# Optimization experiments

Measured on AMD Instinct MI355X. Metric: run time of the kernel, lower is better.

Reference implementation:

```python
import jax, jax.numpy as jnp
import numpy as np
from jax import lax

NUM_DISP = 64
BLOCK = 21
EPS = 1e-12  # F.normalize default eps


def _box_sum(v):
    # v: (N, H, W) -> BLOCK x BLOCK zero-padded box sum (same shape), separable.
    p = BLOCK // 2
    v = v[:, None]  # (N,1,H,W)
    kv = jnp.ones((1, 1, BLOCK, 1), v.dtype)
    kh = jnp.ones((1, 1, 1, BLOCK), v.dtype)
    v = lax.conv_general_dilated(v, kv, (1, 1), ((p, p), (0, 0)))
    v = lax.conv_general_dilated(v, kh, (1, 1), ((0, 0), (p, p)))
    return v[:, 0]


def _l2norm_c(img):
    n = jnp.sqrt(jnp.sum(img * img, axis=1, keepdims=True))
    return img / jnp.maximum(n, EPS)


def _disparity(left, right):
    # left, right: (B, 3, H, W)
    left = _l2norm_c(left)
    right = _l2norm_c(right)
    B, C, H, W = left.shape
    d = jnp.arange(NUM_DISP)
    xs = jnp.arange(W)
    idx = xs[None, :] - d[:, None]              # (D, W): source column in right image
    valid = (idx >= 0)
    r_shift = right[:, :, :, jnp.clip(idx, 0)]  # (B, C, H, D, W)
    r_shift = jnp.where(valid[None, None, None], r_shift, 0.0)
    # per-pixel channel-summed absolute difference -> (B, D, H, W)
    diff = jnp.sum(jnp.abs(left[:, :, :, None, :] - r_shift), axis=1)  # (B, H, D, W)
    diff = jnp.transpose(diff, (0, 2, 1, 3))    # (B, D, H, W)
    cost = _box_sum(diff.reshape(B * NUM_DISP, H, W)).reshape(B, NUM_DISP, H, W)
    cost = cost / (C * BLOCK * BLOCK)           # mean SAD over block elements
    return jnp.argmin(cost, axis=1).astype(left.dtype)  # (B, H, W)


def setup_inputs() -> dict:
    key = jax.random.key(0)
    k1, k2 = jax.random.split(key)
    x = jax.random.normal(k1, (2, 6, 320, 512), dtype=jnp.float32)
    gt = jax.random.normal(k2, (2, 6, 320, 512), dtype=jnp.float32)
    return {"x": x, "gt": gt}


def reference(x, gt):
    disp_gt = _disparity(gt[:, :3], gt[:, 3:])
    disp_pred = _disparity(x[:, :3], x[:, 3:])
    return jnp.mean(jnp.abs(disp_pred - disp_gt))
```

## Files before the change

### kernel.cpp

```cpp
#include <hip/hip_runtime.h>
#include <math.h>

constexpr int B = 2, H = 320, W = 512, D = 64;
constexpr int HW = H * W;
constexpr int R = 10;
constexpr int SEG = 80;
constexpr int NSEG = H / SEG;
constexpr int RS = 548;
constexpr float EPS = 1e-12f;

__global__ void k_norm(const float* __restrict__ x, const float* __restrict__ gt,
                       float4* __restrict__ nrm4) {
    int idx = blockIdx.x * blockDim.x + threadIdx.x;
    if (idx >= 2 * B * HW) return;
    int t = idx / (B * HW);
    int rem = idx - t * (B * HW);
    int b = rem / HW;
    int hw = rem - b * HW;
    const float* p = (t == 0 ? x : gt) + (size_t)b * 6 * HW + hw;
    float v0 = p[0],      v1 = p[HW],     v2 = p[2 * HW];
    float v3 = p[3 * HW], v4 = p[4 * HW], v5 = p[5 * HW];
    float n1 = fmaxf(sqrtf(v0 * v0 + v1 * v1 + v2 * v2), EPS);
    float n2 = fmaxf(sqrtf(v3 * v3 + v4 * v4 + v5 * v5), EPS);
    float4* q = nrm4 + (size_t)(t * B + b) * 2 * HW + hw;
    q[0]  = make_float4(v0 / n1, v1 / n1, v2 / n1, 0.f);
    q[HW] = make_float4(v3 / n2, v4 / n2, v5 / n2, 0.f);
}

template<bool FUSE>
__global__ __launch_bounds__(512, 2) void k_cost(const float4* __restrict__ nrm4,
                                                 float* __restrict__ cost,
                                                 const float* __restrict__ cprev,
                                                 float* __restrict__ dprev, int t) {
    const int blk = blockIdx.x;
    const int combo = blk & 7;
    const int d = blk >> 3;
    const int b = combo >> 2;
    const int seg = combo & 3;
    const int w = threadIdx.x;
    const float4* L4 = nrm4 + (size_t)(t * B + b) * 2 * HW;
    const float4* R4 = L4 + HW;
    const bool val = (w >= d);
    const int wr = val ? (w - d) : 0;
    const int h0 = seg * SEG;

    __shared__ float vsb[2][8][RS];
    {
        int j = w >> 6, k = w & 63;
        if (k < 10)      { vsb[0][j][k] = 0.f;       vsb[1][j][k] = 0.f; }
        else if (k < 20) { vsb[0][j][512 + k] = 0.f; vsb[1][j][512 + k] = 0.f; }
    }

    auto diff = [&](int h) -> float {
        float4 l = L4[(size_t)h * W + w];
        float4 r = R4[(size_t)h * W + wr];
        float a = fabsf(l.x - r.x) + fabsf(l.y - r.y) + fabsf(l.z - r.z);
        float s = fabsf(l.x) + fabsf(l.y) + fabsf(l.z);
        return val ? a : s;
    };

    float ring[24];
    float vs = 0.f;
#pragma unroll
    for (int k = 0; k < 20; ++k) {
        int h = h0 - R + k;
        float dv = (h >= 0) ? diff(h) : 0.f;
        ring[k] = dv;
        vs += dv;
    }
    ring[20] = 0.f; ring[21] = 0.f; ring[22] = 0.f; ring[23] = 0.f;

    const float* cp0 = nullptr; const float* cp1 = nullptr;
    int px0 = 0, px1 = 0;
    float best0 = 3.4e38f, best1 = 3.4e38f;
    int bd0 = 0, bd1 = 0;
    if (FUSE) {
        px0 = blk * 640 + w;
        int b0 = (px0 >= HW) ? 1 : 0;
        cp0 = cprev + (size_t)b0 * D * HW + (px0 - b0 * HW);
        if (w < 128) {
            px1 = blk * 640 + 512 + w;
            int b1 = (px1 >= HW) ? 1 : 0;
            cp1 = cprev + (size_t)b1 * D * HW + (px1 - b1 * HW);
        }
    }

    const int cc = threadIdx.x >> 3;
    const int jj = threadIdx.x & 7;
    float* cp = cost + ((size_t)(b * D + d) * H) * W;

    int dc = 0;
#pragma unroll
    for (int ss = 0; ss < 10; ++ss) {
        const int nd = (ss < 4) ? 7 : 6;
        float dvv[8];
#pragma unroll
        for (int j = 0; j < 8; ++j) {
            int hn = h0 + ss * 8 + j + R;
            dvv[j] = (hn < H) ? diff(hn) : 0.f;
        }
        float fv0[7], fv1[7];
        if (FUSE) {
#pragma unroll
            for (int q = 0; q < 7; ++q)
                if (q < nd) fv0[q] = cp0[(size_t)(dc + q) * HW];
            if (w < 128) {
#pragma unroll
                for (int q = 0; q < 7; ++q)
                    if (q < nd) fv1[q] = cp1[(size_t)(dc + q) * HW];
            }
        }
        float* vrow = &vsb[ss & 1][0][0];
#pragma unroll
        for (int j = 0; j < 8; ++j) {
            int i = ss * 8 + j;
            vs += dvv[j] - ring[(i + 23) % 24];
            ring[(i + 20) % 24] = dvv[j];
            vrow[j * RS + 10 + w] = vs;
        }
        __syncthreads();
        const float* vp = &vsb[ss & 1][jj][8 * cc];
        float wnd[28];
#pragma unroll
        for (int q = 0; q < 7; ++q) {
            float4 v4 = *(const float4*)(vp + 4 * q);
            wnd[4 * q] = v4.x; wnd[4 * q + 1] = v4.y;
            wnd[4 * q + 2] = v4.z; wnd[4 * q + 3] = v4.w;
        }
        float o = 0.f;
#pragma unroll
        for (int k = 0; k < 21; ++k) o += wnd[k];
        float out[8];
        out[0] = o;
#pragma unroll
        for (int k = 1; k < 8; ++k) { o += wnd[20 + k] - wnd[k - 1]; out[k] = o; }
        float* op = cp + (size_t)(h0 + ss * 8 + jj) * W + 8 * cc;
        *(float4*)(op)     = make_float4(out[0], out[1], out[2], out[3]);
        *(float4*)(op + 4) = make_float4(out[4], out[5], out[6], out[7]);
        if (FUSE) {
#pragma unroll
            for (int q = 0; q < 7; ++q)
                if (q < nd && fv0[q] < best0) { best0 = fv0[q]; bd0 = dc + q; }
            if (w < 128) {
#pragma unroll
                for (int q = 0; q < 7; ++q)
                    if (q < nd && fv1[q] < best1) { best1 = fv1[q]; bd1 = dc + q; }
            }
        }
        dc += nd;
    }
    if (FUSE) {
        dprev[px0] = (float)bd0;
        if (w < 128) dprev[px1] = (float)bd1;
    }
}

__global__ void k_argmin0(const float* __restrict__ cost, float* __restrict__ disp) {
    int idx = blockIdx.x * 256 + threadIdx.x;
    if (idx >= B * HW) return;
    int b = (idx >= HW) ? 1 : 0;
    const float* cp = cost + (size_t)b * D * HW + (idx - b * HW);
    float best = cp[0]; int bd = 0;
#pragma unroll 8
    for (int d = 1; d < D; ++d) {
        float v = cp[(size_t)d * HW];
        if (v < best) { best = v; bd = d; }
    }
    disp[idx] = (float)bd;
}

__global__ void k_final(const float* __restrict__ cost1, const float* __restrict__ disp0,
                        float* __restrict__ part) {
    int idx = blockIdx.x * 256 + threadIdx.x;
    float s = 0.f;
    if (idx < B * HW) {
        int b = (idx >= HW) ? 1 : 0;
        const float* cp = cost1 + (size_t)b * D * HW + (idx - b * HW);
        float best = cp[0]; int bd = 0;
#pragma unroll 8
        for (int d = 1; d < D; ++d) {
            float v = cp[(size_t)d * HW];
            if (v < best) { best = v; bd = d; }
        }
        s = fabsf((float)bd - disp0[idx]);
    }
    __shared__ float sm[256];
    sm[threadIdx.x] = s;
    __syncthreads();
    for (int off = 128; off; off >>= 1) {
        if (threadIdx.x < off) sm[threadIdx.x] += sm[threadIdx.x + off];
        __syncthreads();
    }
    if (!threadIdx.x) part[blockIdx.x] = sm[0];
}

__global__ void k_red2(const float* __restrict__ part, float* __restrict__ out,
                       int nb, float inv) {
    __shared__ float sm[256];
    int tid = threadIdx.x;
    float s = 0.f;
    for (int i = tid; i < nb; i += 256) s += part[i];
    sm[tid] = s;
    __syncthreads();
    for (int off = 128; off; off >>= 1) {
        if (tid < off) sm[tid] += sm[tid + off];
        __syncthreads();
    }
    if (!tid) out[0] = sm[0] * inv;
}

extern "C" void kernel_launch(void* const* d_in, const int* in_sizes, int n_in,
                              void* d_out, int out_size, void* d_ws, size_t ws_size,
                              hipStream_t stream) {
    const float* x  = (const float*)d_in[0];
    const float* gt = (const float*)d_in[1];

    constexpr size_t NRM_F4 = (size_t)2 * B * 2 * HW;
    constexpr size_t COST_F = (size_t)B * D * HW;
    constexpr int NPIX_BLKS = (B * HW + 255) / 256;
    constexpr int NRM_BLKS  = (2 * B * HW + 255) / 256;

    float4* nrm4 = (float4*)d_ws;
    float* cost0 = (float*)(nrm4 + NRM_F4);

    size_t need_primary = NRM_F4 * 16 + 2 * COST_F * 4 + (size_t)(B * HW + 4096) * 4;

    k_norm<<<NRM_BLKS, 256, 0, stream>>>(x, gt, nrm4);

    if (ws_size >= need_primary) {
        float* cost1 = cost0 + COST_F;
        float* disp0 = cost1 + COST_F;
        float* part  = disp0 + (size_t)B * HW;
        k_cost<false><<<B * NSEG * D, 512, 0, stream>>>(nrm4, cost0, nullptr, nullptr, 0);
        k_cost<true><<<B * NSEG * D, 512, 0, stream>>>(nrm4, cost1, cost0, disp0, 1);
        k_final<<<NPIX_BLKS, 256, 0, stream>>>(cost1, disp0, part);
        k_red2<<<1, 256, 0, stream>>>(part, (float*)d_out, NPIX_BLKS, 1.f / (float)(B * HW));
    } else {
        float* disp0 = cost0 + COST_F;
        float* part  = disp0 + (size_t)B * HW;
        k_cost<false><<<B * NSEG * D, 512, 0, stream>>>(nrm4, cost0, nullptr, nullptr, 0);
        k_argmin0<<<NPIX_BLKS, 256, 0, stream>>>(cost0, disp0);
        k_cost<false><<<B * NSEG * D, 512, 0, stream>>>(nrm4, cost0, nullptr, nullptr, 1);
        k_final<<<NPIX_BLKS, 256, 0, stream>>>(cost0, disp0, part);
        k_red2<<<1, 256, 0, stream>>>(part, (float*)d_out, NPIX_BLKS, 1.f / (float)(B * HW));
    }
}
```

Measured before the change: 198.4 us.

## Vectorize norm and argmin kernels, move cost ring buffer to shared memory

```diff
diff --git a/kernel.cpp b/kernel.cpp
--- a/kernel.cpp
+++ b/kernel.cpp
@@ -11,20 +11,30 @@
 
 __global__ void k_norm(const float* __restrict__ x, const float* __restrict__ gt,
                        float4* __restrict__ nrm4) {
-    int idx = blockIdx.x * blockDim.x + threadIdx.x;
-    if (idx >= 2 * B * HW) return;
-    int t = idx / (B * HW);
-    int rem = idx - t * (B * HW);
-    int b = rem / HW;
-    int hw = rem - b * HW;
-    const float* p = (t == 0 ? x : gt) + (size_t)b * 6 * HW + hw;
-    float v0 = p[0],      v1 = p[HW],     v2 = p[2 * HW];
-    float v3 = p[3 * HW], v4 = p[4 * HW], v5 = p[5 * HW];
-    float n1 = fmaxf(sqrtf(v0 * v0 + v1 * v1 + v2 * v2), EPS);
-    float n2 = fmaxf(sqrtf(v3 * v3 + v4 * v4 + v5 * v5), EPS);
-    float4* q = nrm4 + (size_t)(t * B + b) * 2 * HW + hw;
-    q[0]  = make_float4(v0 / n1, v1 / n1, v2 / n1, 0.f);
-    q[HW] = make_float4(v3 / n2, v4 / n2, v5 / n2, 0.f);
+    int idx = blockIdx.x * 256 + threadIdx.x;
+    if (idx >= 2 * B * (HW / 4)) return;
+    int t = idx / (B * (HW / 4));
+    int rem = idx - t * (B * (HW / 4));
+    int b = rem / (HW / 4);
+    int hw4 = rem - b * (HW / 4);
+    const float* p = (t == 0 ? x : gt) + (size_t)b * 6 * HW + 4 * hw4;
+    float4 c[6];
+#pragma unroll
+    for (int ch = 0; ch < 6; ++ch) c[ch] = *(const float4*)(p + (size_t)ch * HW);
+    float4* q = nrm4 + (size_t)(t * B + b) * 2 * HW + 4 * hw4;
+    float4 o0[4], o1[4];
+    const float* cf = (const float*)c;
+#pragma unroll
+    for (int k = 0; k < 4; ++k) {
+        float v0 = cf[k], v1 = cf[4 + k], v2 = cf[8 + k];
+        float v3 = cf[12 + k], v4 = cf[16 + k], v5 = cf[20 + k];
+        float n1 = fmaxf(sqrtf(v0 * v0 + v1 * v1 + v2 * v2), EPS);
+        float n2 = fmaxf(sqrtf(v3 * v3 + v4 * v4 + v5 * v5), EPS);
+        o0[k] = make_float4(v0 / n1, v1 / n1, v2 / n1, 0.f);
+        o1[k] = make_float4(v3 / n2, v4 / n2, v5 / n2, 0.f);
+    }
+#pragma unroll
+    for (int k = 0; k < 4; ++k) { q[k] = o0[k]; q[HW + k] = o1[k]; }
 }
 
 template<bool FUSE>
@@ -44,6 +54,7 @@
     const int wr = val ? (w - d) : 0;
     const int h0 = seg * SEG;
 
+    __shared__ float ring[21][W];
     __shared__ float vsb[2][8][RS];
     {
         int j = w >> 6, k = w & 63;
@@ -53,22 +64,21 @@
 
     auto diff = [&](int h) -> float {
         float4 l = L4[(size_t)h * W + w];
-        float4 r = R4[(size_t)h * W + wr];
-        float a = fabsf(l.x - r.x) + fabsf(l.y - r.y) + fabsf(l.z - r.z);
-        float s = fabsf(l.x) + fabsf(l.y) + fabsf(l.z);
-        return val ? a : s;
+        if (val) {
+            float4 r = R4[(size_t)h * W + wr];
+            return fabsf(l.x - r.x) + fabsf(l.y - r.y) + fabsf(l.z - r.z);
+        }
+        return fabsf(l.x) + fabsf(l.y) + fabsf(l.z);
     };
 
-    float ring[24];
     float vs = 0.f;
-#pragma unroll
     for (int k = 0; k < 20; ++k) {
         int h = h0 - R + k;
-        float dv = (h >= 0) ? diff(h) : 0.f;
-        ring[k] = dv;
-        vs += dv;
-    }
-    ring[20] = 0.f; ring[21] = 0.f; ring[22] = 0.f; ring[23] = 0.f;
+        float dv0 = (h >= 0) ? diff(h) : 0.f;
+        ring[k][w] = dv0;
+        vs += dv0;
+    }
+    ring[20][w] = 0.f;
 
     const float* cp0 = nullptr; const float* cp1 = nullptr;
     int px0 = 0, px1 = 0;
@@ -89,15 +99,20 @@
     const int jj = threadIdx.x & 7;
     float* cp = cost + ((size_t)(b * D + d) * H) * W;
 
+    int slot0 = 20;
     int dc = 0;
-#pragma unroll
     for (int ss = 0; ss < 10; ++ss) {
         const int nd = (ss < 4) ? 7 : 6;
-        float dvv[8];
+        int sl[8];
+        float dold[8], dv[8];
+#pragma unroll
+        for (int j = 0; j < 8; ++j) { int s2 = slot0 + j; if (s2 >= 21) s2 -= 21; sl[j] = s2; }
+#pragma unroll
+        for (int j = 0; j < 8; ++j) dold[j] = ring[sl[j]][w];
 #pragma unroll
         for (int j = 0; j < 8; ++j) {
             int hn = h0 + ss * 8 + j + R;
-            dvv[j] = (hn < H) ? diff(hn) : 0.f;
+            dv[j] = (hn < H) ? diff(hn) : 0.f;
         }
         float fv0[7], fv1[7];
         if (FUSE) {
@@ -110,14 +125,11 @@
                     if (q < nd) fv1[q] = cp1[(size_t)(dc + q) * HW];
             }
         }
+#pragma unroll
+        for (int j = 0; j < 8; ++j) ring[sl[j]][w] = dv[j];
         float* vrow = &vsb[ss & 1][0][0];
 #pragma unroll
-        for (int j = 0; j < 8; ++j) {
-            int i = ss * 8 + j;
-            vs += dvv[j] - ring[(i + 23) % 24];
-            ring[(i + 20) % 24] = dvv[j];
-            vrow[j * RS + 10 + w] = vs;
-        }
+        for (int j = 0; j < 8; ++j) { vs += dv[j] - dold[j]; vrow[j * RS + 10 + w] = vs; }
         __syncthreads();
         const float* vp = &vsb[ss & 1][jj][8 * cc];
         float wnd[28];
@@ -148,6 +160,7 @@
             }
         }
         dc += nd;
+        slot0 += 8; if (slot0 >= 21) slot0 -= 21;
     }
     if (FUSE) {
         dprev[px0] = (float)bd0;
@@ -155,35 +168,44 @@
     }
 }
 
-__global__ void k_argmin0(const float* __restrict__ cost, float* __restrict__ disp) {
-    int idx = blockIdx.x * 256 + threadIdx.x;
-    if (idx >= B * HW) return;
-    int b = (idx >= HW) ? 1 : 0;
-    const float* cp = cost + (size_t)b * D * HW + (idx - b * HW);
-    float best = cp[0]; int bd = 0;
-#pragma unroll 8
+__global__ void k_amin(const float* __restrict__ cost, float* __restrict__ disp) {
+    int blk = blockIdx.x;
+    int b = (blk * 1024 >= HW) ? 1 : 0;
+    int hw0 = blk * 1024 - b * HW + threadIdx.x * 4;
+    const float* cp = cost + (size_t)b * D * HW + hw0;
+    float4 v = *(const float4*)cp;
+    float bb[4] = {v.x, v.y, v.z, v.w};
+    int bd[4] = {0, 0, 0, 0};
     for (int d = 1; d < D; ++d) {
-        float v = cp[(size_t)d * HW];
-        if (v < best) { best = v; bd = d; }
-    }
-    disp[idx] = (float)bd;
-}
-
-__global__ void k_final(const float* __restrict__ cost1, const float* __restrict__ disp0,
-                        float* __restrict__ part) {
-    int idx = blockIdx.x * 256 + threadIdx.x;
-    float s = 0.f;
-    if (idx < B * HW) {
-        int b = (idx >= HW) ? 1 : 0;
-        const float* cp = cost1 + (size_t)b * D * HW + (idx - b * HW);
-        float best = cp[0]; int bd = 0;
-#pragma unroll 8
-        for (int d = 1; d < D; ++d) {
-            float v = cp[(size_t)d * HW];
-            if (v < best) { best = v; bd = d; }
-        }
-        s = fabsf((float)bd - disp0[idx]);
-    }
+        v = *(const float4*)(cp + (size_t)d * HW);
+        if (v.x < bb[0]) { bb[0] = v.x; bd[0] = d; }
+        if (v.y < bb[1]) { bb[1] = v.y; bd[1] = d; }
+        if (v.z < bb[2]) { bb[2] = v.z; bd[2] = d; }
+        if (v.w < bb[3]) { bb[3] = v.w; bd[3] = d; }
+    }
+    *(float4*)(disp + (size_t)blk * 1024 + threadIdx.x * 4) =
+        make_float4((float)bd[0], (float)bd[1], (float)bd[2], (float)bd[3]);
+}
+
+__global__ void k_fin(const float* __restrict__ cost1, const float* __restrict__ disp0,
+                      float* __restrict__ part) {
+    int blk = blockIdx.x;
+    int b = (blk * 1024 >= HW) ? 1 : 0;
+    int hw0 = blk * 1024 - b * HW + threadIdx.x * 4;
+    const float* cp = cost1 + (size_t)b * D * HW + hw0;
+    float4 v = *(const float4*)cp;
+    float bb[4] = {v.x, v.y, v.z, v.w};
+    int bd[4] = {0, 0, 0, 0};
+    for (int d = 1; d < D; ++d) {
+        v = *(const float4*)(cp + (size_t)d * HW);
+        if (v.x < bb[0]) { bb[0] = v.x; bd[0] = d; }
+        if (v.y < bb[1]) { bb[1] = v.y; bd[1] = d; }
+        if (v.z < bb[2]) { bb[2] = v.z; bd[2] = d; }
+        if (v.w < bb[3]) { bb[3] = v.w; bd[3] = d; }
+    }
+    float4 d0 = *(const float4*)(disp0 + (size_t)blk * 1024 + threadIdx.x * 4);
+    float s = fabsf((float)bd[0] - d0.x) + fabsf((float)bd[1] - d0.y) +
+              fabsf((float)bd[2] - d0.z) + fabsf((float)bd[3] - d0.w);
     __shared__ float sm[256];
     sm[threadIdx.x] = s;
     __syncthreads();
@@ -217,8 +239,8 @@
 
     constexpr size_t NRM_F4 = (size_t)2 * B * 2 * HW;
     constexpr size_t COST_F = (size_t)B * D * HW;
-    constexpr int NPIX_BLKS = (B * HW + 255) / 256;
-    constexpr int NRM_BLKS  = (2 * B * HW + 255) / 256;
+    constexpr int AMIN_BLKS = B * HW / 1024;
+    constexpr int NRM_BLKS  = (2 * B * (HW / 4) + 255) / 256;
 
     float4* nrm4 = (float4*)d_ws;
     float* cost0 = (float*)(nrm4 + NRM_F4);
@@ -233,15 +255,15 @@
         float* part  = disp0 + (size_t)B * HW;
         k_cost<false><<<B * NSEG * D, 512, 0, stream>>>(nrm4, cost0, nullptr, nullptr, 0);
         k_cost<true><<<B * NSEG * D, 512, 0, stream>>>(nrm4, cost1, cost0, disp0, 1);
-        k_final<<<NPIX_BLKS, 256, 0, stream>>>(cost1, disp0, part);
-        k_red2<<<1, 256, 0, stream>>>(part, (float*)d_out, NPIX_BLKS, 1.f / (float)(B * HW));
+        k_fin<<<AMIN_BLKS, 256, 0, stream>>>(cost1, disp0, part);
+        k_red2<<<1, 256, 0, stream>>>(part, (float*)d_out, AMIN_BLKS, 1.f / (float)(B * HW));
     } else {
         float* disp0 = cost0 + COST_F;
         float* part  = disp0 + (size_t)B * HW;
         k_cost<false><<<B * NSEG * D, 512, 0, stream>>>(nrm4, cost0, nullptr, nullptr, 0);
-        k_argmin0<<<NPIX_BLKS, 256, 0, stream>>>(cost0, disp0);
+        k_amin<<<AMIN_BLKS, 256, 0, stream>>>(cost0, disp0);
         k_cost<false><<<B * NSEG * D, 512, 0, stream>>>(nrm4, cost0, nullptr, nullptr, 1);
-        k_final<<<NPIX_BLKS, 256, 0, stream>>>(cost0, disp0, part);
-        k_red2<<<1, 256, 0, stream>>>(part, (float*)d_out, NPIX_BLKS, 1.f / (float)(B * HW));
-    }
-}
+        k_fin<<<AMIN_BLKS, 256, 0, stream>>>(cost0, disp0, part);
+        k_red2<<<1, 256, 0, stream>>>(part, (float*)d_out, AMIN_BLKS, 1.f / (float)(B * HW));
+    }
+}
```

Result: faster. 193.6 us (-2.4%).
